# Kernel optimization log

Measured on AMD Instinct MI355X. Metric: run time of the kernel, lower is better.

Reference implementation:

```python
import jax, jax.numpy as jnp
import numpy as np

N_ATOMS = 100_000
N_PAIRS = 6_400_000
CUTOFF = 5.0
CUTON = 4.0


def setup_inputs() -> dict:
    key = jax.random.key(0)
    k = jax.random.split(key, 4)
    atomic_numbers = jax.random.uniform(k[0], (N_ATOMS,), jnp.float32, 1.0, 94.0)
    displacements = jax.random.normal(k[1], (N_PAIRS, 3), jnp.float32) * 2.0
    idx_i = jnp.sort(jax.random.randint(k[2], (N_PAIRS,), 0, N_ATOMS, jnp.int32))
    idx_j = jax.random.randint(k[3], (N_PAIRS,), 0, N_ATOMS, jnp.int32)
    atom_mask = jnp.ones((N_ATOMS,), jnp.float32)
    batch_segments = jnp.zeros((N_ATOMS,), jnp.int32)
    batch_mask = jnp.ones((N_PAIRS,), jnp.float32)
    # ZBL parameters (non-trainable constants from setup())
    a_coefficient = jnp.asarray(0.8854, jnp.float32)
    a_exponent = jnp.asarray(0.23, jnp.float32)
    phi_coefficients = jnp.array([0.18175, 0.50986, 0.28022, 0.02817], jnp.float32)
    phi_exponents = jnp.array([3.1998, 0.94229, 0.4029, 0.20162], jnp.float32)
    return dict(
        atomic_numbers=atomic_numbers,
        displacements=displacements,
        idx_i=idx_i,
        idx_j=idx_j,
        atom_mask=atom_mask,
        batch_segments=batch_segments,
        batch_mask=batch_mask,
        batch_size=1,
        a_coefficient=a_coefficient,
        a_exponent=a_exponent,
        phi_coefficients=phi_coefficients,
        phi_exponents=phi_exponents,
    )


def _switch_fn(distances):
    # smooth 1 -> 0 switch between CUTON and CUTOFF
    x = (CUTOFF - distances) / (CUTOFF - CUTON)
    poly = ((6.0 * x - 15.0) * x + 10.0) * x ** 3
    return jnp.where(distances < CUTON, 1.0, jnp.where(distances >= CUTOFF, 0.0, poly))


def reference(atomic_numbers, displacements, idx_i, idx_j, atom_mask,
              batch_segments, batch_mask, batch_size,
              a_coefficient, a_exponent, phi_coefficients, phi_exponents):
    distances = jnp.maximum(jnp.linalg.norm(displacements, axis=-1), 1e-10)  # [E]
    switch_off = _switch_fn(distances)

    za = jnp.power(atomic_numbers, jnp.abs(a_exponent))  # [N]
    denominator = jnp.maximum(za[idx_i] + za[idx_j], 1e-10)  # [E]
    a_ij = jnp.abs(a_coefficient) / denominator
    arguments = distances / a_ij  # [E]

    coefficients = jax.nn.softmax(jnp.abs(phi_coefficients))  # [4]
    exponents = jnp.abs(phi_exponents)  # [4]
    log_terms = -exponents[None, :] * arguments[:, None]  # [E,4]
    max_log = jnp.max(log_terms, axis=1, keepdims=True)
    # NOTE: faithful to the original -- max_log is never added back
    phi = jnp.sum(coefficients[None, :] * jnp.exp(log_terms - max_log), axis=1)  # [E]

    log_repulsion = (jnp.log(0.5)
                     + jnp.log(atomic_numbers[idx_i])
                     + jnp.log(atomic_numbers[idx_j])
                     - jnp.log(distances)
                     + jnp.log(jnp.maximum(phi, 1e-30))
                     + jnp.log(jnp.maximum(switch_off, 1e-30)))
    repulsion = jnp.exp(log_repulsion) * batch_mask  # [E]

    Erep = jax.ops.segment_sum(repulsion, segment_ids=idx_i,
                               num_segments=atomic_numbers.shape[0])  # [N]
    Erep = Erep * atom_mask
    return Erep[..., None, None, None]
```

## Files before the change

kernel.cpp:

```cpp
#include <hip/hip_runtime.h>
#include <math.h>

#define LOG2E 1.4426950408889634f
#define NSLOT 512
#define EPB   1024


__global__ __launch_bounds__(256) void zbl_prep_kernel(
    const float* __restrict__ z, const float* __restrict__ amask,
    const float* __restrict__ a_coef, const float* __restrict__ a_exp,
    const float* __restrict__ phi_c, const float* __restrict__ phi_e,
    float2* __restrict__ tab_i, float2* __restrict__ tab_j,
    float* __restrict__ out, float* __restrict__ consts, int n_atoms) {
  int n = blockIdx.x * blockDim.x + threadIdx.x;
  if (n < n_atoms) {
    float zi = z[n];
    float ae = fabsf(a_exp[0]);
    float za = __builtin_amdgcn_exp2f(ae * __builtin_amdgcn_logf(zi));
    tab_i[n] = make_float2(za, 0.5f * zi * amask[n]);
    tab_j[n] = make_float2(za, zi);
    out[n] = 0.0f;
  }
  if (blockIdx.x == 0 && threadIdx.x == 0) {
    float c[4], e2[4];
    float m = -1e30f;
    for (int k = 0; k < 4; ++k) { c[k] = fabsf(phi_c[k]); m = fmaxf(m, c[k]); }
    float s = 0.0f;
    for (int k = 0; k < 4; ++k) { c[k] = expf(c[k] - m); s += c[k]; }
    for (int k = 0; k < 4; ++k) c[k] /= s;
    int kmin = 0;
    for (int k = 0; k < 4; ++k) {
      e2[k] = fabsf(phi_e[k]) * LOG2E;
      if (e2[k] < e2[kmin]) kmin = k;
    }
    float inv_a = 1.0f / fabsf(a_coef[0]);
    consts[0] = c[kmin];
    int p = 1;
    for (int k = 0; k < 4; ++k) {
      if (k != kmin) {
        consts[p] = c[k];
        consts[3 + p] = (e2[k] - e2[kmin]) * inv_a;
        ++p;
      }
    }
  }
}

__device__ __forceinline__ float zbl_edge_value(
    float dx, float dy, float dz, float2 ti, float2 tj, float bm,
    float c0, float c1, float c2, float c3,
    float dd1, float dd2, float dd3) {
  float n2 = fmaxf(dx * dx + dy * dy + dz * dz, 1e-20f);
  float r = __builtin_amdgcn_rsqf(n2);
  float d = n2 * r;
  float x = 5.0f - d;
  float poly = ((6.0f * x - 15.0f) * x + 10.0f) * x * x * x;
  float sw = (d < 4.0f) ? 1.0f : ((d >= 5.0f) ? 0.0f : poly);
  float q = d * fmaxf(ti.x + tj.x, 1e-10f);
  float phi = c0 + c1 * __builtin_amdgcn_exp2f(-dd1 * q)
                 + c2 * __builtin_amdgcn_exp2f(-dd2 * q)
                 + c3 * __builtin_amdgcn_exp2f(-dd3 * q);
  return ti.y * tj.y * r * fmaxf(phi, 1e-30f) * fmaxf(sw, 1e-30f) * bm;
}

__global__ __launch_bounds__(256, 8) void zbl_edge_kernel(
    const float* __restrict__ disp, const int* __restrict__ idx_i,
    const int* __restrict__ idx_j, const float* __restrict__ bmask,
    const float2* __restrict__ tab_i, const float2* __restrict__ tab_j,
    const float* __restrict__ consts, float* __restrict__ out, int n_edges) {
  __shared__ float acc[NSLOT];
  const int t = threadIdx.x;
  const long block_base = (long)blockIdx.x * EPB;

  acc[t] = 0.0f;
  acc[t + 256] = 0.0f;

  const int key_base = idx_i[block_base];
  const float c0 = consts[0], c1 = consts[1], c2 = consts[2], c3 = consts[3];
  const float dd1 = consts[4], dd2 = consts[5], dd3 = consts[6];

  const long L = (long)blockIdx.x * 256 + t;
  const long e0 = L * 4;

  int k0 = -1, k1 = -1, k2 = -1, k3 = -1;
  float v0 = 0.f, v1 = 0.f, v2 = 0.f, v3 = 0.f;

  if (e0 + 3 < (long)n_edges) {
    int4 I = ((const int4*)idx_i)[L];
    int4 J = ((const int4*)idx_j)[L];
    const float4* d4 = (const float4*)disp;
    float4 A = d4[3 * L], B = d4[3 * L + 1], Cc = d4[3 * L + 2];
    float4 BM = ((const float4*)bmask)[L];
    float2 ti0 = tab_i[I.x], ti1 = tab_i[I.y], ti2 = tab_i[I.z], ti3 = tab_i[I.w];
    float2 tj0 = tab_j[J.x], tj1 = tab_j[J.y], tj2 = tab_j[J.z], tj3 = tab_j[J.w];
    v0 = zbl_edge_value(A.x, A.y, A.z, ti0, tj0, BM.x, c0, c1, c2, c3, dd1, dd2, dd3);
    v1 = zbl_edge_value(A.w, B.x, B.y, ti1, tj1, BM.y, c0, c1, c2, c3, dd1, dd2, dd3);
    v2 = zbl_edge_value(B.z, B.w, Cc.x, ti2, tj2, BM.z, c0, c1, c2, c3, dd1, dd2, dd3);
    v3 = zbl_edge_value(Cc.y, Cc.z, Cc.w, ti3, tj3, BM.w, c0, c1, c2, c3, dd1, dd2, dd3);
    k0 = I.x; k1 = I.y; k2 = I.z; k3 = I.w;
  } else {
    long e;
    e = e0;
    if (e < (long)n_edges) {
      int i = idx_i[e], j = idx_j[e];
      v0 = zbl_edge_value(disp[3 * e], disp[3 * e + 1], disp[3 * e + 2],
                          tab_i[i], tab_j[j], bmask[e], c0, c1, c2, c3, dd1, dd2, dd3);
      k0 = i;
    }
    e = e0 + 1;
    if (e < (long)n_edges) {
      int i = idx_i[e], j = idx_j[e];
      v1 = zbl_edge_value(disp[3 * e], disp[3 * e + 1], disp[3 * e + 2],
                          tab_i[i], tab_j[j], bmask[e], c0, c1, c2, c3, dd1, dd2, dd3);
      k1 = i;
    }
    e = e0 + 2;
    if (e < (long)n_edges) {
      int i = idx_i[e], j = idx_j[e];
      v2 = zbl_edge_value(disp[3 * e], disp[3 * e + 1], disp[3 * e + 2],
                          tab_i[i], tab_j[j], bmask[e], c0, c1, c2, c3, dd1, dd2, dd3);
      k2 = i;
    }
    e = e0 + 3;
    if (e < (long)n_edges) {
      int i = idx_i[e], j = idx_j[e];
      v3 = zbl_edge_value(disp[3 * e], disp[3 * e + 1], disp[3 * e + 2],
                          tab_i[i], tab_j[j], bmask[e], c0, c1, c2, c3, dd1, dd2, dd3);
      k3 = i;
    }
  }

  __syncthreads();

  auto flush = [&](int key, float s) {
    if (key < 0) return;
    int slot = key - key_base;
    if ((unsigned)slot < (unsigned)NSLOT) atomicAdd(&acc[slot], s);
    else atomicAdd(&out[key], s);
  };

  {
    int cur = k0;
    float s = v0;
    if (k1 == cur) s += v1; else { flush(cur, s); cur = k1; s = v1; }
    if (k2 == cur) s += v2; else { flush(cur, s); cur = k2; s = v2; }
    if (k3 == cur) s += v3; else { flush(cur, s); cur = k3; s = v3; }
    flush(cur, s);
  }

  __syncthreads();

  #pragma unroll
  for (int s2 = 0; s2 < NSLOT; s2 += 256) {
    float val = acc[t + s2];
    if (val != 0.0f) {
      atomicAdd(&out[key_base + t + s2], val);
    }
  }
}

extern "C" void kernel_launch(void* const* d_in, const int* in_sizes, int n_in,
                              void* d_out, int out_size, void* d_ws,
                              size_t ws_size, hipStream_t stream) {
  const float* atomic_numbers = (const float*)d_in[0];
  const float* disp           = (const float*)d_in[1];
  const int*   idx_i          = (const int*)d_in[2];
  const int*   idx_j          = (const int*)d_in[3];
  const float* atom_mask      = (const float*)d_in[4];
  const float* bmask          = (const float*)d_in[6];
  const float* a_coef         = (const float*)d_in[8];
  const float* a_exp          = (const float*)d_in[9];
  const float* phi_c          = (const float*)d_in[10];
  const float* phi_e          = (const float*)d_in[11];

  int n_atoms = in_sizes[0];
  int n_edges = in_sizes[2];

  float* out = (float*)d_out;
  float2* tab_i = (float2*)d_ws;
  float2* tab_j = (float2*)((char*)d_ws + (size_t)n_atoms * sizeof(float2));
  float* consts = (float*)((char*)d_ws + 2 * (size_t)n_atoms * sizeof(float2));

  int atom_blocks = (n_atoms + 255) / 256;
  int edge_blocks = (int)(((long)n_edges + EPB - 1) / EPB);

  zbl_prep_kernel<<<atom_blocks, 256, 0, stream>>>(
      atomic_numbers, atom_mask, a_coef, a_exp, phi_c, phi_e, tab_i, tab_j,
      out, consts, n_atoms);
  zbl_edge_kernel<<<edge_blocks, 256, 0, stream>>>(
      disp, idx_i, idx_j, bmask, tab_i, tab_j, consts, out, n_edges);
}
```

Measured before the change: 48.44 us.

## Stage per-block source-atom table in shared memory and defer i-factor to flush

Replaces the per-edge gathers of the i-atom table with a shared-memory copy of za for the block's contiguous range of source atoms, which is possible because idx_i is sorted. The per-atom factor 0.5*z_i*mask is pulled out of the per-edge product and applied once per segment when partial sums are flushed. This removes four random 8-byte gathers per thread in exchange for extra shared-memory staging, a second barrier-dependent phase, and an L2 fallback gather for keys outside the 512-slot window.

```diff
diff --git a/kernel.cpp b/kernel.cpp
--- a/kernel.cpp
+++ b/kernel.cpp
@@ -10,15 +10,16 @@
     const float* __restrict__ z, const float* __restrict__ amask,
     const float* __restrict__ a_coef, const float* __restrict__ a_exp,
     const float* __restrict__ phi_c, const float* __restrict__ phi_e,
-    float2* __restrict__ tab_i, float2* __restrict__ tab_j,
+    float2* __restrict__ tabj, float* __restrict__ za, float* __restrict__ fi,
     float* __restrict__ out, float* __restrict__ consts, int n_atoms) {
   int n = blockIdx.x * blockDim.x + threadIdx.x;
   if (n < n_atoms) {
     float zi = z[n];
     float ae = fabsf(a_exp[0]);
-    float za = __builtin_amdgcn_exp2f(ae * __builtin_amdgcn_logf(zi));
-    tab_i[n] = make_float2(za, 0.5f * zi * amask[n]);
-    tab_j[n] = make_float2(za, zi);
+    float zan = __builtin_amdgcn_exp2f(ae * __builtin_amdgcn_logf(zi));
+    tabj[n] = make_float2(zan, zi);
+    za[n] = zan;
+    fi[n] = 0.5f * zi * amask[n];
     out[n] = 0.0f;
   }
   if (blockIdx.x == 0 && threadIdx.x == 0) {
@@ -47,7 +48,7 @@
 }
 
 __device__ __forceinline__ float zbl_edge_value(
-    float dx, float dy, float dz, float2 ti, float2 tj, float bm,
+    float dx, float dy, float dz, float za_i, float2 tj, float bm,
     float c0, float c1, float c2, float c3,
     float dd1, float dd2, float dd3) {
   float n2 = fmaxf(dx * dx + dy * dy + dz * dz, 1e-20f);
@@ -56,26 +57,31 @@
   float x = 5.0f - d;
   float poly = ((6.0f * x - 15.0f) * x + 10.0f) * x * x * x;
   float sw = (d < 4.0f) ? 1.0f : ((d >= 5.0f) ? 0.0f : poly);
-  float q = d * fmaxf(ti.x + tj.x, 1e-10f);
+  float q = d * fmaxf(za_i + tj.x, 1e-10f);
   float phi = c0 + c1 * __builtin_amdgcn_exp2f(-dd1 * q)
                  + c2 * __builtin_amdgcn_exp2f(-dd2 * q)
                  + c3 * __builtin_amdgcn_exp2f(-dd3 * q);
-  return ti.y * tj.y * r * fmaxf(phi, 1e-30f) * fmaxf(sw, 1e-30f) * bm;
+  return tj.y * r * fmaxf(phi, 1e-30f) * fmaxf(sw, 1e-30f) * bm;
 }
 
 __global__ __launch_bounds__(256, 8) void zbl_edge_kernel(
     const float* __restrict__ disp, const int* __restrict__ idx_i,
     const int* __restrict__ idx_j, const float* __restrict__ bmask,
-    const float2* __restrict__ tab_i, const float2* __restrict__ tab_j,
-    const float* __restrict__ consts, float* __restrict__ out, int n_edges) {
+    const float2* __restrict__ tabj, const float* __restrict__ za,
+    const float* __restrict__ fi, const float* __restrict__ consts,
+    float* __restrict__ out, int n_edges, int n_atoms) {
   __shared__ float acc[NSLOT];
+  __shared__ float za_s[NSLOT];
   const int t = threadIdx.x;
-  const long block_base = (long)blockIdx.x * EPB;
-
-  acc[t] = 0.0f;
-  acc[t + 256] = 0.0f;
-
-  const int key_base = idx_i[block_base];
+  const long bb = (long)blockIdx.x * EPB;
+
+  const int key_base = idx_i[bb];
+
+  const int a0 = min(key_base + t, n_atoms - 1);
+  const int a1 = min(key_base + t + 256, n_atoms - 1);
+  const float zs0 = za[a0], zs1 = za[a1];
+  const float fi0 = fi[a0], fi1 = fi[a1];
+
   const float c0 = consts[0], c1 = consts[1], c2 = consts[2], c3 = consts[3];
   const float dd1 = consts[4], dd2 = consts[5], dd3 = consts[6];
 
@@ -83,60 +89,79 @@
   const long e0 = L * 4;
 
   int k0 = -1, k1 = -1, k2 = -1, k3 = -1;
-  float v0 = 0.f, v1 = 0.f, v2 = 0.f, v3 = 0.f;
+  float d00 = 0.f, d01 = 0.f, d02 = 0.f, bm0 = 0.f;
+  float d10 = 0.f, d11 = 0.f, d12 = 0.f, bm1 = 0.f;
+  float d20 = 0.f, d21 = 0.f, d22 = 0.f, bm2 = 0.f;
+  float d30 = 0.f, d31 = 0.f, d32 = 0.f, bm3 = 0.f;
+  float2 tj0 = make_float2(0.f, 0.f), tj1 = tj0, tj2 = tj0, tj3 = tj0;
 
   if (e0 + 3 < (long)n_edges) {
     int4 I = ((const int4*)idx_i)[L];
     int4 J = ((const int4*)idx_j)[L];
+    tj0 = tabj[J.x]; tj1 = tabj[J.y]; tj2 = tabj[J.z]; tj3 = tabj[J.w];
     const float4* d4 = (const float4*)disp;
     float4 A = d4[3 * L], B = d4[3 * L + 1], Cc = d4[3 * L + 2];
     float4 BM = ((const float4*)bmask)[L];
-    float2 ti0 = tab_i[I.x], ti1 = tab_i[I.y], ti2 = tab_i[I.z], ti3 = tab_i[I.w];
-    float2 tj0 = tab_j[J.x], tj1 = tab_j[J.y], tj2 = tab_j[J.z], tj3 = tab_j[J.w];
-    v0 = zbl_edge_value(A.x, A.y, A.z, ti0, tj0, BM.x, c0, c1, c2, c3, dd1, dd2, dd3);
-    v1 = zbl_edge_value(A.w, B.x, B.y, ti1, tj1, BM.y, c0, c1, c2, c3, dd1, dd2, dd3);
-    v2 = zbl_edge_value(B.z, B.w, Cc.x, ti2, tj2, BM.z, c0, c1, c2, c3, dd1, dd2, dd3);
-    v3 = zbl_edge_value(Cc.y, Cc.z, Cc.w, ti3, tj3, BM.w, c0, c1, c2, c3, dd1, dd2, dd3);
+    d00 = A.x;  d01 = A.y;  d02 = A.z;  bm0 = BM.x;
+    d10 = A.w;  d11 = B.x;  d12 = B.y;  bm1 = BM.y;
+    d20 = B.z;  d21 = B.w;  d22 = Cc.x; bm2 = BM.z;
+    d30 = Cc.y; d31 = Cc.z; d32 = Cc.w; bm3 = BM.w;
     k0 = I.x; k1 = I.y; k2 = I.z; k3 = I.w;
   } else {
     long e;
     e = e0;
     if (e < (long)n_edges) {
-      int i = idx_i[e], j = idx_j[e];
-      v0 = zbl_edge_value(disp[3 * e], disp[3 * e + 1], disp[3 * e + 2],
-                          tab_i[i], tab_j[j], bmask[e], c0, c1, c2, c3, dd1, dd2, dd3);
-      k0 = i;
+      k0 = idx_i[e]; tj0 = tabj[idx_j[e]];
+      d00 = disp[3 * e]; d01 = disp[3 * e + 1]; d02 = disp[3 * e + 2];
+      bm0 = bmask[e];
     }
     e = e0 + 1;
     if (e < (long)n_edges) {
-      int i = idx_i[e], j = idx_j[e];
-      v1 = zbl_edge_value(disp[3 * e], disp[3 * e + 1], disp[3 * e + 2],
-                          tab_i[i], tab_j[j], bmask[e], c0, c1, c2, c3, dd1, dd2, dd3);
-      k1 = i;
+      k1 = idx_i[e]; tj1 = tabj[idx_j[e]];
+      d10 = disp[3 * e]; d11 = disp[3 * e + 1]; d12 = disp[3 * e + 2];
+      bm1 = bmask[e];
     }
     e = e0 + 2;
     if (e < (long)n_edges) {
-      int i = idx_i[e], j = idx_j[e];
-      v2 = zbl_edge_value(disp[3 * e], disp[3 * e + 1], disp[3 * e + 2],
-                          tab_i[i], tab_j[j], bmask[e], c0, c1, c2, c3, dd1, dd2, dd3);
-      k2 = i;
+      k2 = idx_i[e]; tj2 = tabj[idx_j[e]];
+      d20 = disp[3 * e]; d21 = disp[3 * e + 1]; d22 = disp[3 * e + 2];
+      bm2 = bmask[e];
     }
     e = e0 + 3;
     if (e < (long)n_edges) {
-      int i = idx_i[e], j = idx_j[e];
-      v3 = zbl_edge_value(disp[3 * e], disp[3 * e + 1], disp[3 * e + 2],
-                          tab_i[i], tab_j[j], bmask[e], c0, c1, c2, c3, dd1, dd2, dd3);
-      k3 = i;
-    }
-  }
-
+      k3 = idx_i[e]; tj3 = tabj[idx_j[e]];
+      d30 = disp[3 * e]; d31 = disp[3 * e + 1]; d32 = disp[3 * e + 2];
+      bm3 = bmask[e];
+    }
+  }
+
+  acc[t] = 0.0f;
+  acc[t + 256] = 0.0f;
+  za_s[t] = zs0;
+  za_s[t + 256] = zs1;
   __syncthreads();
+
+  auto za_i = [&](int i) -> float {
+    if (i < 0) return 0.0f;
+    int s = i - key_base;
+    if ((unsigned)s < (unsigned)NSLOT) return za_s[s];
+    return za[i];
+  };
+
+  float v0 = (k0 >= 0) ? zbl_edge_value(d00, d01, d02, za_i(k0), tj0, bm0,
+                                        c0, c1, c2, c3, dd1, dd2, dd3) : 0.f;
+  float v1 = (k1 >= 0) ? zbl_edge_value(d10, d11, d12, za_i(k1), tj1, bm1,
+                                        c0, c1, c2, c3, dd1, dd2, dd3) : 0.f;
+  float v2 = (k2 >= 0) ? zbl_edge_value(d20, d21, d22, za_i(k2), tj2, bm2,
+                                        c0, c1, c2, c3, dd1, dd2, dd3) : 0.f;
+  float v3 = (k3 >= 0) ? zbl_edge_value(d30, d31, d32, za_i(k3), tj3, bm3,
+                                        c0, c1, c2, c3, dd1, dd2, dd3) : 0.f;
 
   auto flush = [&](int key, float s) {
     if (key < 0) return;
     int slot = key - key_base;
     if ((unsigned)slot < (unsigned)NSLOT) atomicAdd(&acc[slot], s);
-    else atomicAdd(&out[key], s);
+    else atomicAdd(&out[key], s * fi[key]);
   };
 
   {
@@ -150,12 +175,11 @@
 
   __syncthreads();
 
-  #pragma unroll
-  for (int s2 = 0; s2 < NSLOT; s2 += 256) {
-    float val = acc[t + s2];
-    if (val != 0.0f) {
-      atomicAdd(&out[key_base + t + s2], val);
-    }
+  {
+    float val = acc[t];
+    if (val != 0.0f) atomicAdd(&out[key_base + t], val * fi0);
+    val = acc[t + 256];
+    if (val != 0.0f) atomicAdd(&out[key_base + t + 256], val * fi1);
   }
 }
 
@@ -177,16 +201,18 @@
   int n_edges = in_sizes[2];
 
   float* out = (float*)d_out;
-  float2* tab_i = (float2*)d_ws;
-  float2* tab_j = (float2*)((char*)d_ws + (size_t)n_atoms * sizeof(float2));
-  float* consts = (float*)((char*)d_ws + 2 * (size_t)n_atoms * sizeof(float2));
+  float2* tabj = (float2*)d_ws;
+  float*  zaw  = (float*)((char*)d_ws + (size_t)n_atoms * sizeof(float2));
+  float*  fiw  = zaw + n_atoms;
+  float*  consts = fiw + n_atoms;
 
   int atom_blocks = (n_atoms + 255) / 256;
   int edge_blocks = (int)(((long)n_edges + EPB - 1) / EPB);
 
   zbl_prep_kernel<<<atom_blocks, 256, 0, stream>>>(
-      atomic_numbers, atom_mask, a_coef, a_exp, phi_c, phi_e, tab_i, tab_j,
+      atomic_numbers, atom_mask, a_coef, a_exp, phi_c, phi_e, tabj, zaw, fiw,
       out, consts, n_atoms);
   zbl_edge_kernel<<<edge_blocks, 256, 0, stream>>>(
-      disp, idx_i, idx_j, bmask, tab_i, tab_j, consts, out, n_edges);
-}
+      disp, idx_i, idx_j, bmask, tabj, zaw, fiw, consts, out, n_edges,
+      n_atoms);
+}
```

Measured after the change: 50.02 us. 3.2% more time.
